# Optimization experiments

Hardware: AMD Instinct MI355X
Metric: run time of the kernel (lower is better)

## Reference

```python
import jax, jax.numpy as jnp
import numpy as np

N_NODES = 40000
N_EDGES = 640000
IN_CH = 128
HID_CH = 256
EDGE_DIM = 64
N_SAMP = 2048
T = 1.0
EPS_GIN = 0.0
EPS_NORM = 1e-12


def setup_inputs() -> dict:
    key = jax.random.key(0)
    ks = jax.random.split(key, 12)
    x = jax.random.normal(ks[0], (N_NODES, IN_CH), dtype=jnp.float32)
    edge_index = jax.random.randint(ks[1], (2, N_EDGES), 0, N_NODES, dtype=jnp.int64)
    edge_attr = jax.random.normal(ks[2], (N_EDGES, EDGE_DIM), dtype=jnp.float32)
    pos_ind = jax.random.randint(ks[3], (N_SAMP,), 0, N_NODES, dtype=jnp.int64)
    neg_ind = jax.random.randint(ks[4], (N_SAMP,), 0, N_NODES, dtype=jnp.int64)
    # GINEConv internal edge projection Linear(64 -> 128)
    We = jax.random.normal(ks[5], (EDGE_DIM, IN_CH), dtype=jnp.float32) / np.sqrt(EDGE_DIM)
    be = jnp.zeros((IN_CH,), dtype=jnp.float32)
    # MLP: Linear(128->256), ReLU, Linear(256->256)
    W1 = jax.random.normal(ks[6], (IN_CH, HID_CH), dtype=jnp.float32) / np.sqrt(IN_CH)
    b1 = jnp.zeros((HID_CH,), dtype=jnp.float32)
    W2 = jax.random.normal(ks[7], (HID_CH, HID_CH), dtype=jnp.float32) / np.sqrt(HID_CH)
    b2 = jnp.zeros((HID_CH,), dtype=jnp.float32)
    thresholding_node = jax.random.normal(ks[8], (1, HID_CH), dtype=jnp.float32)
    return {"x": x, "edge_index": edge_index, "edge_attr": edge_attr,
            "pos_ind": pos_ind, "neg_ind": neg_ind,
            "We": We, "be": be, "W1": W1, "b1": b1, "W2": W2, "b2": b2,
            "thresholding_node": thresholding_node}


def _normalize(v):
    n = jnp.linalg.norm(v, axis=-1, keepdims=True)
    return v / jnp.maximum(n, EPS_NORM)


def reference(x, edge_index, edge_attr, pos_ind, neg_ind,
              We, be, W1, b1, W2, b2, thresholding_node):
    src, dst = edge_index[0], edge_index[1]  # PyG: message from x_j (src) to target i (dst)
    edge_emb = edge_attr @ We + be                    # [E, in_ch]
    msg = jax.nn.relu(x[src] + edge_emb)              # gather + add + relu
    agg = jax.ops.segment_sum(msg, dst, num_segments=x.shape[0])  # scatter-add
    h = (1.0 + EPS_GIN) * x + agg
    emb = jax.nn.relu(h @ W1 + b1) @ W2 + b2          # [N, hid]

    center = _normalize(emb[0])                       # [hid]
    pos = _normalize(emb[pos_ind])                    # [P, hid]
    neg = _normalize(emb[neg_ind])                    # [Q, hid]
    thr = _normalize(thresholding_node)               # [1, hid]

    pos_score_mean = (center[None, :] * pos).sum(-1).mean(-1)
    neg_score_mean = (center[None, :] * neg).sum(-1).mean(-1)
    thr_score = (center * thr).sum(-1)                # [1]

    pos_loss = jnp.log(jnp.clip(jax.nn.sigmoid((pos_score_mean - thr_score) / T), 1e-12)).mean()
    neg_loss = jnp.log(jnp.clip(jax.nn.sigmoid((thr_score - neg_score_mean) / T), 1e-12)).mean()
    return -pos_loss - neg_loss
```

## Files before the change

kernel.cpp:

```cpp
#include <hip/hip_runtime.h>
#include <math.h>

#define N_NODES 40000
#define N_EDGES 640000
#define IN_CH 128
#define HID_CH 256
#define EDGE_DIM 64
#define N_SAMP 2048
#define NSEL (1 + 2 * N_SAMP)
#define MAXU 4097
#define HBUCKETS 5120

__global__ __launch_bounds__(256) void init_kernel(
    int* __restrict__ slot, int* __restrict__ counters,
    int* __restrict__ hist, float4* __restrict__ agg4)
{
    const int i = blockIdx.x * 256 + threadIdx.x;
    const int n = gridDim.x * 256;
    for (int j = i; j < 40960; j += n) slot[j] = -1;
    for (int j = i; j < HBUCKETS; j += n) hist[j] = 0;
    for (int j = i; j < 32; j += n) counters[j] = 0;
    const float4 z = make_float4(0.f, 0.f, 0.f, 0.f);
    for (int j = i; j < (MAXU * IN_CH) / 4; j += n) agg4[j] = z;
}

__global__ __launch_bounds__(256) void flag_kernel(
    const int* __restrict__ pos, const int* __restrict__ neg,
    int* __restrict__ slot, int* __restrict__ counters)
{
    int r = blockIdx.x * 256 + threadIdx.x;
    if (r >= NSEL) return;
    int node = (r == 0) ? 0 : (r <= N_SAMP ? pos[r - 1] : neg[r - 1 - N_SAMP]);
    int old = atomicCAS(&slot[node], -1, -2);
    if (old == -1) slot[node] = atomicAdd(&counters[1], 1);
}

__global__ __launch_bounds__(256) void compact_kernel(
    const int* __restrict__ ei, const int* __restrict__ slot,
    int* __restrict__ counters, int* __restrict__ hist, int4* __restrict__ cmp)
{
    const int tid = threadIdx.x, wave = tid >> 6, lane = tid & 63;
    const int e = blockIdx.x * 256 + tid;
    const int d = ei[N_EDGES + e];
    const int sl = slot[d];
    const bool valid = (sl >= 0);
    unsigned long long m = __ballot(valid);
    int wrank = __popcll(m & ((1ULL << lane) - 1ULL));
    __shared__ int woff[4];
    __shared__ int bbase;
    if (lane == 0) woff[wave] = __popcll(m);
    __syncthreads();
    if (tid == 0) {
        int t = 0;
        for (int i = 0; i < 4; ++i) { int c = woff[i]; woff[i] = t; t += c; }
        bbase = atomicAdd(&counters[0], t);
    }
    __syncthreads();
    if (valid) {
        int idx = bbase + woff[wave] + wrank;
        cmp[idx] = make_int4(e, ei[e], sl, 0);
        atomicAdd(&hist[sl], 1);
    }
}

__global__ __launch_bounds__(1024) void scan_kernel(
    const int* __restrict__ hist, int* __restrict__ cursor)
{
    __shared__ int tmp[1024];
    const int t = threadIdx.x;
    int v[5]; int s = 0;
#pragma unroll
    for (int i = 0; i < 5; ++i) { v[i] = hist[t * 5 + i]; s += v[i]; }
    tmp[t] = s;
    __syncthreads();
    for (int d = 1; d < 1024; d <<= 1) {
        int a = (t >= d) ? tmp[t - d] : 0;
        __syncthreads();
        tmp[t] += a;
        __syncthreads();
    }
    int run = tmp[t] - s;
#pragma unroll
    for (int i = 0; i < 5; ++i) { cursor[t * 5 + i] = run; run += v[i]; }
}

__global__ __launch_bounds__(256) void scatter_kernel(
    const int4* __restrict__ cmp, const int* __restrict__ counters,
    int* __restrict__ cursor, int4* __restrict__ sorted)
{
    const int M = counters[0];
    for (int i = blockIdx.x * 256 + threadIdx.x; i < M; i += gridDim.x * 256) {
        int4 c = cmp[i];
        int p = atomicAdd(&cursor[c.z], 1);
        sorted[p] = c;
    }
}

__global__ __launch_bounds__(256) void edge_kernel(
    const float* __restrict__ x, const float* __restrict__ edge_attr,
    const float* __restrict__ We, const float* __restrict__ be,
    const int* __restrict__ counters, const int4* __restrict__ sorted,
    float* __restrict__ agg_c)
{
    __shared__ float sWe[EDGE_DIM * IN_CH];
    __shared__ float sAttr[4][16 * EDGE_DIM];
    __shared__ int sE[4][16], sS[4][16], sL[4][16];
    const int tid = threadIdx.x, wave = tid >> 6, lane = tid & 63;
    const int M = counters[0];

    {
        const float4* s4 = (const float4*)We;
        float4* d4 = (float4*)sWe;
        for (int i = tid; i < (EDGE_DIM * IN_CH) / 4; i += 256) d4[i] = s4[i];
    }
    __syncthreads();
    const float be0 = be[lane], be1 = be[64 + lane];

    for (int b = blockIdx.x * 64; b < M; b += gridDim.x * 64) {
        const int wb = b + wave * 16;
        if (lane < 16) {
            int idx = wb + lane;
            bool v = idx < M;
            int4 c = sorted[v ? idx : 0];
            sE[wave][lane] = c.x;
            sS[wave][lane] = c.y;
            sL[wave][lane] = v ? c.z : -1;
        }
        __syncthreads();
        {
            int sub = lane >> 4, q = lane & 15;
#pragma unroll
            for (int p = 0; p < 4; ++p) {
                int j = p * 4 + sub;
                int e = sE[wave][j];
                ((float4*)&sAttr[wave][j * EDGE_DIM])[q] =
                    ((const float4*)(edge_attr + (size_t)e * EDGE_DIM))[q];
            }
        }
        __syncthreads();

        float acc0[16], acc1[16];
#pragma unroll
        for (int j = 0; j < 16; ++j) { acc0[j] = 0.f; acc1[j] = 0.f; }
        for (int k0 = 0; k0 < EDGE_DIM; k0 += 4) {
            float w0[4], w1[4];
#pragma unroll
            for (int kk = 0; kk < 4; ++kk) {
                w0[kk] = sWe[(k0 + kk) * IN_CH + lane];
                w1[kk] = sWe[(k0 + kk) * IN_CH + 64 + lane];
            }
#pragma unroll
            for (int j = 0; j < 16; ++j) {
                float4 a = *(const float4*)&sAttr[wave][j * EDGE_DIM + k0];
                acc0[j] += a.x * w0[0] + a.y * w0[1] + a.z * w0[2] + a.w * w0[3];
                acc1[j] += a.x * w1[0] + a.y * w1[1] + a.z * w1[2] + a.w * w1[3];
            }
        }

        float sum0 = 0.f, sum1 = 0.f;
#pragma unroll
        for (int j = 0; j < 16; ++j) {
            int sl = sL[wave][j];
            if (sl >= 0) {
                int s = sS[wave][j];
                float m0 = fmaxf(x[(size_t)s * IN_CH + lane] + acc0[j] + be0, 0.f);
                float m1 = fmaxf(x[(size_t)s * IN_CH + 64 + lane] + acc1[j] + be1, 0.f);
                sum0 += m0;
                sum1 += m1;
                bool flush = (j == 15) || (sL[wave][j + 1] != sl);
                if (flush) {
                    atomicAdd(&agg_c[(size_t)sl * IN_CH + lane], sum0);
                    atomicAdd(&agg_c[(size_t)sl * IN_CH + 64 + lane], sum1);
                    sum0 = 0.f;
                    sum1 = 0.f;
                }
            }
        }
        __syncthreads();
    }
}

__global__ __launch_bounds__(256) void mlp_kernel(
    const float* __restrict__ x, const float* __restrict__ agg_c,
    const int* __restrict__ slot, const int* __restrict__ pos,
    const int* __restrict__ neg, const float* __restrict__ W1,
    const float* __restrict__ b1, const float* __restrict__ W2,
    const float* __restrict__ b2, float* __restrict__ emb)
{
    __shared__ float sin_[16][IN_CH];
    __shared__ float shid[16][HID_CH];
    __shared__ int snode[16], sslot[16];
    const int tid = threadIdx.x;
    const int r0 = blockIdx.x * 16;
    if (tid < 16) {
        int r = r0 + tid;
        int node = 0;
        if (r < NSEL && r > 0) node = (r <= N_SAMP) ? pos[r - 1] : neg[r - 1 - N_SAMP];
        snode[tid] = node;
        sslot[tid] = slot[node];
    }
    __syncthreads();
    for (int i = tid; i < 16 * (IN_CH / 4); i += 256) {
        int rr = i >> 5, k4 = i & 31;
        int n = snode[rr], sl = sslot[rr];
        float4 xa = ((const float4*)(x + (size_t)n * IN_CH))[k4];
        float4 ga = ((const float4*)(agg_c + (size_t)sl * IN_CH))[k4];
        ((float4*)sin_[rr])[k4] =
            make_float4(xa.x + ga.x, xa.y + ga.y, xa.z + ga.z, xa.w + ga.w);
    }
    __syncthreads();

    float acc[16];
#pragma unroll
    for (int rr = 0; rr < 16; ++rr) acc[rr] = 0.f;
    for (int k0 = 0; k0 < IN_CH; k0 += 4) {
        float w[4];
#pragma unroll
        for (int kk = 0; kk < 4; ++kk) w[kk] = W1[(k0 + kk) * HID_CH + tid];
#pragma unroll
        for (int rr = 0; rr < 16; ++rr) {
            float4 h = *(const float4*)&sin_[rr][k0];
            acc[rr] += h.x * w[0] + h.y * w[1] + h.z * w[2] + h.w * w[3];
        }
    }
    float bb1 = b1[tid];
#pragma unroll
    for (int rr = 0; rr < 16; ++rr) shid[rr][tid] = fmaxf(acc[rr] + bb1, 0.f);
    __syncthreads();

#pragma unroll
    for (int rr = 0; rr < 16; ++rr) acc[rr] = 0.f;
    for (int k0 = 0; k0 < HID_CH; k0 += 4) {
        float w[4];
#pragma unroll
        for (int kk = 0; kk < 4; ++kk) w[kk] = W2[(k0 + kk) * HID_CH + tid];
#pragma unroll
        for (int rr = 0; rr < 16; ++rr) {
            float4 h = *(const float4*)&shid[rr][k0];
            acc[rr] += h.x * w[0] + h.y * w[1] + h.z * w[2] + h.w * w[3];
        }
    }
    float bb2 = b2[tid];
#pragma unroll
    for (int rr = 0; rr < 16; ++rr) {
        int r = r0 + rr;
        if (r < NSEL) emb[(size_t)r * HID_CH + tid] = acc[rr] + bb2;
    }
}

__global__ __launch_bounds__(256) void score_kernel(
    const float* __restrict__ emb, float* __restrict__ partial)
{
    const int tid = threadIdx.x;
    const int wave = tid >> 6, lane = tid & 63;
    const int rid = blockIdx.x * 4 + wave;
    const float4 c = ((const float4*)emb)[lane];
    const float4 v = ((const float4*)(emb + (size_t)(rid + 1) * HID_CH))[lane];
    float cc = c.x * c.x + c.y * c.y + c.z * c.z + c.w * c.w;
    float vv = v.x * v.x + v.y * v.y + v.z * v.z + v.w * v.w;
    float cv = c.x * v.x + c.y * v.y + c.z * v.z + c.w * v.w;
#pragma unroll
    for (int off = 32; off; off >>= 1) {
        cc += __shfl_xor(cc, off, 64);
        vv += __shfl_xor(vv, off, 64);
        cv += __shfl_xor(cv, off, 64);
    }
    float score = cv / (fmaxf(sqrtf(cc), 1e-12f) * fmaxf(sqrtf(vv), 1e-12f));
    __shared__ float wsum[4];
    if (lane == 0) wsum[wave] = score;
    __syncthreads();
    if (tid == 0) partial[blockIdx.x] = wsum[0] + wsum[1] + wsum[2] + wsum[3];
}

__global__ __launch_bounds__(64) void loss_kernel(
    const float* __restrict__ emb, const float* __restrict__ thrn,
    const float* __restrict__ partial, float* __restrict__ out)
{
    const int lane = threadIdx.x;
    const float4 c = ((const float4*)emb)[lane];
    const float4 t = ((const float4*)thrn)[lane];
    float cc = c.x * c.x + c.y * c.y + c.z * c.z + c.w * c.w;
    float tt = t.x * t.x + t.y * t.y + t.z * t.z + t.w * t.w;
    float ct = c.x * t.x + c.y * t.y + c.z * t.z + c.w * t.w;
    float ps = 0.f, ns = 0.f;
#pragma unroll
    for (int i = 0; i < 8; ++i) ps += partial[lane + 64 * i];
#pragma unroll
    for (int i = 0; i < 8; ++i) ns += partial[512 + lane + 64 * i];
#pragma unroll
    for (int off = 32; off; off >>= 1) {
        cc += __shfl_xor(cc, off, 64);
        tt += __shfl_xor(tt, off, 64);
        ct += __shfl_xor(ct, off, 64);
        ps += __shfl_xor(ps, off, 64);
        ns += __shfl_xor(ns, off, 64);
    }
    if (lane == 0) {
        float thr = ct / (fmaxf(sqrtf(cc), 1e-12f) * fmaxf(sqrtf(tt), 1e-12f));
        float pm = ps / (float)N_SAMP;
        float nm = ns / (float)N_SAMP;
        float s1 = 1.f / (1.f + expf(-(pm - thr)));
        float s2 = 1.f / (1.f + expf(-(thr - nm)));
        s1 = fmaxf(s1, 1e-12f);
        s2 = fmaxf(s2, 1e-12f);
        out[0] = -(logf(s1) + logf(s2));
    }
}

extern "C" void kernel_launch(void* const* d_in, const int* in_sizes, int n_in,
                              void* d_out, int out_size, void* d_ws, size_t ws_size,
                              hipStream_t stream)
{
    const float* x         = (const float*)d_in[0];
    const int*   ei        = (const int*)d_in[1];
    const float* edge_attr = (const float*)d_in[2];
    const int*   pos       = (const int*)d_in[3];
    const int*   neg       = (const int*)d_in[4];
    const float* We        = (const float*)d_in[5];
    const float* be        = (const float*)d_in[6];
    const float* W1        = (const float*)d_in[7];
    const float* b1        = (const float*)d_in[8];
    const float* W2        = (const float*)d_in[9];
    const float* b2        = (const float*)d_in[10];
    const float* thrn      = (const float*)d_in[11];
    float* out = (float*)d_out;

    int* slot     = (int*)d_ws;
    int* counters = slot + 40960;
    int* hist     = counters + 32;
    int* cursor   = hist + HBUCKETS;
    int4* cmp     = (int4*)(cursor + HBUCKETS);
    int4* sorted  = cmp + N_EDGES;
    float* agg_c  = (float*)(sorted + N_EDGES);
    float* emb    = agg_c + 524800;
    float* partial= emb + 1048832;

    init_kernel<<<512, 256, 0, stream>>>(slot, counters, hist, (float4*)agg_c);
    flag_kernel<<<(NSEL + 255) / 256, 256, 0, stream>>>(pos, neg, slot, counters);
    compact_kernel<<<N_EDGES / 256, 256, 0, stream>>>(ei, slot, counters, hist, cmp);
    scan_kernel<<<1, 1024, 0, stream>>>(hist, cursor);
    scatter_kernel<<<256, 256, 0, stream>>>(cmp, counters, cursor, sorted);
    edge_kernel<<<1024, 256, 0, stream>>>(x, edge_attr, We, be, counters, sorted, agg_c);
    mlp_kernel<<<(NSEL + 15) / 16, 256, 0, stream>>>(x, agg_c, slot, pos, neg,
                                                     W1, b1, W2, b2, emb);
    score_kernel<<<1024, 256, 0, stream>>>(emb, partial);
    loss_kernel<<<1, 64, 0, stream>>>(emb, thrn, partial, out);
}
```

Baseline: 367.4 us.

## Fuse pipeline into one cooperative persistent kernel and drop edge sorting

After: 919.1 us. 2.5x slower.

```diff
diff --git a/kernel.cpp b/kernel.cpp
--- a/kernel.cpp
+++ b/kernel.cpp
@@ -1,5 +1,8 @@
 #include <hip/hip_runtime.h>
+#include <hip/hip_cooperative_groups.h>
 #include <math.h>
+
+namespace cg = cooperative_groups;
 
 #define N_NODES 40000
 #define N_EDGES 640000
@@ -9,301 +12,270 @@
 #define N_SAMP 2048
 #define NSEL (1 + 2 * N_SAMP)
 #define MAXU 4097
-#define HBUCKETS 5120
-
-__global__ __launch_bounds__(256) void init_kernel(
-    int* __restrict__ slot, int* __restrict__ counters,
-    int* __restrict__ hist, float4* __restrict__ agg4)
+#define GRID 512
+#define BLK 256
+
+struct EdgeSmem {
+    float sWe[EDGE_DIM * IN_CH];
+    float sAttr[4][16 * EDGE_DIM];
+    int sE[4][16], sS[4][16], sL[4][16];
+};
+struct MlpSmem {
+    float sin_[16][IN_CH];
+    float shid[16][HID_CH];
+    int snode[16], sslot[16];
+};
+struct CmpSmem { int woff[4]; int bbase; };
+struct ScSmem { float wsum[4]; };
+
+__global__ __launch_bounds__(BLK) void mega_kernel(
+    const float* __restrict__ x, const int* __restrict__ ei,
+    const float* __restrict__ edge_attr,
+    const int* __restrict__ pos, const int* __restrict__ neg,
+    const float* __restrict__ We, const float* __restrict__ be,
+    const float* __restrict__ W1, const float* __restrict__ b1,
+    const float* __restrict__ W2, const float* __restrict__ b2,
+    const float* __restrict__ thrn,
+    int* slot, int* counters, int4* cmp, float* agg_c,
+    float* emb, float* partial, float* out)
 {
-    const int i = blockIdx.x * 256 + threadIdx.x;
-    const int n = gridDim.x * 256;
-    for (int j = i; j < 40960; j += n) slot[j] = -1;
-    for (int j = i; j < HBUCKETS; j += n) hist[j] = 0;
-    for (int j = i; j < 32; j += n) counters[j] = 0;
-    const float4 z = make_float4(0.f, 0.f, 0.f, 0.f);
-    for (int j = i; j < (MAXU * IN_CH) / 4; j += n) agg4[j] = z;
-}
-
-__global__ __launch_bounds__(256) void flag_kernel(
-    const int* __restrict__ pos, const int* __restrict__ neg,
-    int* __restrict__ slot, int* __restrict__ counters)
-{
-    int r = blockIdx.x * 256 + threadIdx.x;
-    if (r >= NSEL) return;
-    int node = (r == 0) ? 0 : (r <= N_SAMP ? pos[r - 1] : neg[r - 1 - N_SAMP]);
-    int old = atomicCAS(&slot[node], -1, -2);
-    if (old == -1) slot[node] = atomicAdd(&counters[1], 1);
-}
-
-__global__ __launch_bounds__(256) void compact_kernel(
-    const int* __restrict__ ei, const int* __restrict__ slot,
-    int* __restrict__ counters, int* __restrict__ hist, int4* __restrict__ cmp)
-{
+    cg::grid_group grid = cg::this_grid();
+    __shared__ __align__(16) char smem[sizeof(EdgeSmem)];
     const int tid = threadIdx.x, wave = tid >> 6, lane = tid & 63;
-    const int e = blockIdx.x * 256 + tid;
-    const int d = ei[N_EDGES + e];
-    const int sl = slot[d];
-    const bool valid = (sl >= 0);
-    unsigned long long m = __ballot(valid);
-    int wrank = __popcll(m & ((1ULL << lane) - 1ULL));
-    __shared__ int woff[4];
-    __shared__ int bbase;
-    if (lane == 0) woff[wave] = __popcll(m);
-    __syncthreads();
-    if (tid == 0) {
-        int t = 0;
-        for (int i = 0; i < 4; ++i) { int c = woff[i]; woff[i] = t; t += c; }
-        bbase = atomicAdd(&counters[0], t);
-    }
-    __syncthreads();
-    if (valid) {
-        int idx = bbase + woff[wave] + wrank;
-        cmp[idx] = make_int4(e, ei[e], sl, 0);
-        atomicAdd(&hist[sl], 1);
-    }
-}
-
-__global__ __launch_bounds__(1024) void scan_kernel(
-    const int* __restrict__ hist, int* __restrict__ cursor)
-{
-    __shared__ int tmp[1024];
-    const int t = threadIdx.x;
-    int v[5]; int s = 0;
-#pragma unroll
-    for (int i = 0; i < 5; ++i) { v[i] = hist[t * 5 + i]; s += v[i]; }
-    tmp[t] = s;
-    __syncthreads();
-    for (int d = 1; d < 1024; d <<= 1) {
-        int a = (t >= d) ? tmp[t - d] : 0;
+    const int gtid = blockIdx.x * BLK + tid;
+    const int gsz = GRID * BLK;
+
+    for (int j = gtid; j < 40960; j += gsz) slot[j] = -1;
+    if (gtid < 32) counters[gtid] = 0;
+    {
+        float4* agg4 = (float4*)agg_c;
+        const float4 z = make_float4(0.f, 0.f, 0.f, 0.f);
+        for (int j = gtid; j < (MAXU * IN_CH) / 4; j += gsz) agg4[j] = z;
+    }
+    __threadfence();
+    grid.sync();
+
+    for (int r = gtid; r < NSEL; r += gsz) {
+        int node = (r == 0) ? 0 : (r <= N_SAMP ? pos[r - 1] : neg[r - 1 - N_SAMP]);
+        int old = atomicCAS(&slot[node], -1, -2);
+        if (old == -1) slot[node] = atomicAdd(&counters[1], 1);
+    }
+    __threadfence();
+    grid.sync();
+
+    {
+        CmpSmem* cs = (CmpSmem*)smem;
+        for (int base = blockIdx.x * BLK; base < N_EDGES; base += gsz) {
+            int e = base + tid;
+            int d = ei[N_EDGES + e];
+            int sl = slot[d];
+            bool valid = (sl >= 0);
+            unsigned long long m = __ballot(valid);
+            int wrank = __popcll(m & ((1ULL << lane) - 1ULL));
+            if (lane == 0) cs->woff[wave] = __popcll(m);
+            __syncthreads();
+            if (tid == 0) {
+                int t = 0;
+                for (int i = 0; i < 4; ++i) { int c = cs->woff[i]; cs->woff[i] = t; t += c; }
+                cs->bbase = atomicAdd(&counters[0], t);
+            }
+            __syncthreads();
+            if (valid) cmp[cs->bbase + cs->woff[wave] + wrank] = make_int4(e, ei[e], sl, 0);
+            __syncthreads();
+        }
+    }
+    __threadfence();
+    grid.sync();
+
+    {
+        EdgeSmem* es = (EdgeSmem*)smem;
+        const int M = counters[0];
+        {
+            const float4* s4 = (const float4*)We;
+            float4* d4 = (float4*)es->sWe;
+            for (int i = tid; i < (EDGE_DIM * IN_CH) / 4; i += BLK) d4[i] = s4[i];
+        }
         __syncthreads();
-        tmp[t] += a;
-        __syncthreads();
-    }
-    int run = tmp[t] - s;
-#pragma unroll
-    for (int i = 0; i < 5; ++i) { cursor[t * 5 + i] = run; run += v[i]; }
-}
-
-__global__ __launch_bounds__(256) void scatter_kernel(
-    const int4* __restrict__ cmp, const int* __restrict__ counters,
-    int* __restrict__ cursor, int4* __restrict__ sorted)
-{
-    const int M = counters[0];
-    for (int i = blockIdx.x * 256 + threadIdx.x; i < M; i += gridDim.x * 256) {
-        int4 c = cmp[i];
-        int p = atomicAdd(&cursor[c.z], 1);
-        sorted[p] = c;
-    }
-}
-
-__global__ __launch_bounds__(256) void edge_kernel(
-    const float* __restrict__ x, const float* __restrict__ edge_attr,
-    const float* __restrict__ We, const float* __restrict__ be,
-    const int* __restrict__ counters, const int4* __restrict__ sorted,
-    float* __restrict__ agg_c)
-{
-    __shared__ float sWe[EDGE_DIM * IN_CH];
-    __shared__ float sAttr[4][16 * EDGE_DIM];
-    __shared__ int sE[4][16], sS[4][16], sL[4][16];
-    const int tid = threadIdx.x, wave = tid >> 6, lane = tid & 63;
-    const int M = counters[0];
-
-    {
-        const float4* s4 = (const float4*)We;
-        float4* d4 = (float4*)sWe;
-        for (int i = tid; i < (EDGE_DIM * IN_CH) / 4; i += 256) d4[i] = s4[i];
-    }
-    __syncthreads();
-    const float be0 = be[lane], be1 = be[64 + lane];
-
-    for (int b = blockIdx.x * 64; b < M; b += gridDim.x * 64) {
-        const int wb = b + wave * 16;
-        if (lane < 16) {
-            int idx = wb + lane;
-            bool v = idx < M;
-            int4 c = sorted[v ? idx : 0];
-            sE[wave][lane] = c.x;
-            sS[wave][lane] = c.y;
-            sL[wave][lane] = v ? c.z : -1;
-        }
-        __syncthreads();
-        {
-            int sub = lane >> 4, q = lane & 15;
-#pragma unroll
-            for (int p = 0; p < 4; ++p) {
-                int j = p * 4 + sub;
-                int e = sE[wave][j];
-                ((float4*)&sAttr[wave][j * EDGE_DIM])[q] =
-                    ((const float4*)(edge_attr + (size_t)e * EDGE_DIM))[q];
-            }
-        }
-        __syncthreads();
-
-        float acc0[16], acc1[16];
-#pragma unroll
-        for (int j = 0; j < 16; ++j) { acc0[j] = 0.f; acc1[j] = 0.f; }
-        for (int k0 = 0; k0 < EDGE_DIM; k0 += 4) {
-            float w0[4], w1[4];
-#pragma unroll
-            for (int kk = 0; kk < 4; ++kk) {
-                w0[kk] = sWe[(k0 + kk) * IN_CH + lane];
-                w1[kk] = sWe[(k0 + kk) * IN_CH + 64 + lane];
+        const float be0 = be[lane], be1 = be[64 + lane];
+
+        for (int b = blockIdx.x * 64; b < M; b += GRID * 64) {
+            const int wb = b + wave * 16;
+            if (lane < 16) {
+                int idx = wb + lane;
+                bool v = idx < M;
+                int4 c = cmp[v ? idx : 0];
+                es->sE[wave][lane] = c.x;
+                es->sS[wave][lane] = c.y;
+                es->sL[wave][lane] = v ? c.z : -1;
+            }
+            __syncthreads();
+            {
+                int sub = lane >> 4, q = lane & 15;
+#pragma unroll
+                for (int p = 0; p < 4; ++p) {
+                    int j = p * 4 + sub;
+                    int e = es->sE[wave][j];
+                    ((float4*)&es->sAttr[wave][j * EDGE_DIM])[q] =
+                        ((const float4*)(edge_attr + (size_t)e * EDGE_DIM))[q];
+                }
+            }
+            __syncthreads();
+
+            float acc0[16], acc1[16];
+#pragma unroll
+            for (int j = 0; j < 16; ++j) { acc0[j] = 0.f; acc1[j] = 0.f; }
+            for (int k0 = 0; k0 < EDGE_DIM; k0 += 4) {
+                float w0[4], w1[4];
+#pragma unroll
+                for (int kk = 0; kk < 4; ++kk) {
+                    w0[kk] = es->sWe[(k0 + kk) * IN_CH + lane];
+                    w1[kk] = es->sWe[(k0 + kk) * IN_CH + 64 + lane];
+                }
+#pragma unroll
+                for (int j = 0; j < 16; ++j) {
+                    float4 a = *(const float4*)&es->sAttr[wave][j * EDGE_DIM + k0];
+                    acc0[j] += a.x * w0[0] + a.y * w0[1] + a.z * w0[2] + a.w * w0[3];
+                    acc1[j] += a.x * w1[0] + a.y * w1[1] + a.z * w1[2] + a.w * w1[3];
+                }
             }
 #pragma unroll
             for (int j = 0; j < 16; ++j) {
-                float4 a = *(const float4*)&sAttr[wave][j * EDGE_DIM + k0];
-                acc0[j] += a.x * w0[0] + a.y * w0[1] + a.z * w0[2] + a.w * w0[3];
-                acc1[j] += a.x * w1[0] + a.y * w1[1] + a.z * w1[2] + a.w * w1[3];
-            }
-        }
-
-        float sum0 = 0.f, sum1 = 0.f;
-#pragma unroll
-        for (int j = 0; j < 16; ++j) {
-            int sl = sL[wave][j];
-            if (sl >= 0) {
-                int s = sS[wave][j];
-                float m0 = fmaxf(x[(size_t)s * IN_CH + lane] + acc0[j] + be0, 0.f);
-                float m1 = fmaxf(x[(size_t)s * IN_CH + 64 + lane] + acc1[j] + be1, 0.f);
-                sum0 += m0;
-                sum1 += m1;
-                bool flush = (j == 15) || (sL[wave][j + 1] != sl);
-                if (flush) {
-                    atomicAdd(&agg_c[(size_t)sl * IN_CH + lane], sum0);
-                    atomicAdd(&agg_c[(size_t)sl * IN_CH + 64 + lane], sum1);
-                    sum0 = 0.f;
-                    sum1 = 0.f;
-                }
-            }
-        }
-        __syncthreads();
-    }
-}
-
-__global__ __launch_bounds__(256) void mlp_kernel(
-    const float* __restrict__ x, const float* __restrict__ agg_c,
-    const int* __restrict__ slot, const int* __restrict__ pos,
-    const int* __restrict__ neg, const float* __restrict__ W1,
-    const float* __restrict__ b1, const float* __restrict__ W2,
-    const float* __restrict__ b2, float* __restrict__ emb)
-{
-    __shared__ float sin_[16][IN_CH];
-    __shared__ float shid[16][HID_CH];
-    __shared__ int snode[16], sslot[16];
-    const int tid = threadIdx.x;
-    const int r0 = blockIdx.x * 16;
-    if (tid < 16) {
-        int r = r0 + tid;
-        int node = 0;
-        if (r < NSEL && r > 0) node = (r <= N_SAMP) ? pos[r - 1] : neg[r - 1 - N_SAMP];
-        snode[tid] = node;
-        sslot[tid] = slot[node];
-    }
-    __syncthreads();
-    for (int i = tid; i < 16 * (IN_CH / 4); i += 256) {
-        int rr = i >> 5, k4 = i & 31;
-        int n = snode[rr], sl = sslot[rr];
-        float4 xa = ((const float4*)(x + (size_t)n * IN_CH))[k4];
-        float4 ga = ((const float4*)(agg_c + (size_t)sl * IN_CH))[k4];
-        ((float4*)sin_[rr])[k4] =
-            make_float4(xa.x + ga.x, xa.y + ga.y, xa.z + ga.z, xa.w + ga.w);
-    }
-    __syncthreads();
-
-    float acc[16];
-#pragma unroll
-    for (int rr = 0; rr < 16; ++rr) acc[rr] = 0.f;
-    for (int k0 = 0; k0 < IN_CH; k0 += 4) {
-        float w[4];
-#pragma unroll
-        for (int kk = 0; kk < 4; ++kk) w[kk] = W1[(k0 + kk) * HID_CH + tid];
-#pragma unroll
-        for (int rr = 0; rr < 16; ++rr) {
-            float4 h = *(const float4*)&sin_[rr][k0];
-            acc[rr] += h.x * w[0] + h.y * w[1] + h.z * w[2] + h.w * w[3];
-        }
-    }
-    float bb1 = b1[tid];
-#pragma unroll
-    for (int rr = 0; rr < 16; ++rr) shid[rr][tid] = fmaxf(acc[rr] + bb1, 0.f);
-    __syncthreads();
-
-#pragma unroll
-    for (int rr = 0; rr < 16; ++rr) acc[rr] = 0.f;
-    for (int k0 = 0; k0 < HID_CH; k0 += 4) {
-        float w[4];
-#pragma unroll
-        for (int kk = 0; kk < 4; ++kk) w[kk] = W2[(k0 + kk) * HID_CH + tid];
-#pragma unroll
-        for (int rr = 0; rr < 16; ++rr) {
-            float4 h = *(const float4*)&shid[rr][k0];
-            acc[rr] += h.x * w[0] + h.y * w[1] + h.z * w[2] + h.w * w[3];
-        }
-    }
-    float bb2 = b2[tid];
-#pragma unroll
-    for (int rr = 0; rr < 16; ++rr) {
-        int r = r0 + rr;
-        if (r < NSEL) emb[(size_t)r * HID_CH + tid] = acc[rr] + bb2;
-    }
-}
-
-__global__ __launch_bounds__(256) void score_kernel(
-    const float* __restrict__ emb, float* __restrict__ partial)
-{
-    const int tid = threadIdx.x;
-    const int wave = tid >> 6, lane = tid & 63;
-    const int rid = blockIdx.x * 4 + wave;
-    const float4 c = ((const float4*)emb)[lane];
-    const float4 v = ((const float4*)(emb + (size_t)(rid + 1) * HID_CH))[lane];
-    float cc = c.x * c.x + c.y * c.y + c.z * c.z + c.w * c.w;
-    float vv = v.x * v.x + v.y * v.y + v.z * v.z + v.w * v.w;
-    float cv = c.x * v.x + c.y * v.y + c.z * v.z + c.w * v.w;
-#pragma unroll
-    for (int off = 32; off; off >>= 1) {
-        cc += __shfl_xor(cc, off, 64);
-        vv += __shfl_xor(vv, off, 64);
-        cv += __shfl_xor(cv, off, 64);
-    }
-    float score = cv / (fmaxf(sqrtf(cc), 1e-12f) * fmaxf(sqrtf(vv), 1e-12f));
-    __shared__ float wsum[4];
-    if (lane == 0) wsum[wave] = score;
-    __syncthreads();
-    if (tid == 0) partial[blockIdx.x] = wsum[0] + wsum[1] + wsum[2] + wsum[3];
-}
-
-__global__ __launch_bounds__(64) void loss_kernel(
-    const float* __restrict__ emb, const float* __restrict__ thrn,
-    const float* __restrict__ partial, float* __restrict__ out)
-{
-    const int lane = threadIdx.x;
-    const float4 c = ((const float4*)emb)[lane];
-    const float4 t = ((const float4*)thrn)[lane];
-    float cc = c.x * c.x + c.y * c.y + c.z * c.z + c.w * c.w;
-    float tt = t.x * t.x + t.y * t.y + t.z * t.z + t.w * t.w;
-    float ct = c.x * t.x + c.y * t.y + c.z * t.z + c.w * t.w;
-    float ps = 0.f, ns = 0.f;
-#pragma unroll
-    for (int i = 0; i < 8; ++i) ps += partial[lane + 64 * i];
-#pragma unroll
-    for (int i = 0; i < 8; ++i) ns += partial[512 + lane + 64 * i];
-#pragma unroll
-    for (int off = 32; off; off >>= 1) {
-        cc += __shfl_xor(cc, off, 64);
-        tt += __shfl_xor(tt, off, 64);
-        ct += __shfl_xor(ct, off, 64);
-        ps += __shfl_xor(ps, off, 64);
-        ns += __shfl_xor(ns, off, 64);
-    }
-    if (lane == 0) {
-        float thr = ct / (fmaxf(sqrtf(cc), 1e-12f) * fmaxf(sqrtf(tt), 1e-12f));
-        float pm = ps / (float)N_SAMP;
-        float nm = ns / (float)N_SAMP;
-        float s1 = 1.f / (1.f + expf(-(pm - thr)));
-        float s2 = 1.f / (1.f + expf(-(thr - nm)));
-        s1 = fmaxf(s1, 1e-12f);
-        s2 = fmaxf(s2, 1e-12f);
-        out[0] = -(logf(s1) + logf(s2));
+                int sl = es->sL[wave][j];
+                if (sl >= 0) {
+                    int s = es->sS[wave][j];
+                    float m0 = fmaxf(x[(size_t)s * IN_CH + lane] + acc0[j] + be0, 0.f);
+                    float m1 = fmaxf(x[(size_t)s * IN_CH + 64 + lane] + acc1[j] + be1, 0.f);
+                    atomicAdd(&agg_c[(size_t)sl * IN_CH + lane], m0);
+                    atomicAdd(&agg_c[(size_t)sl * IN_CH + 64 + lane], m1);
+                }
+            }
+            __syncthreads();
+        }
+    }
+    __threadfence();
+    grid.sync();
+
+    {
+        MlpSmem* ms = (MlpSmem*)smem;
+        for (int tile = blockIdx.x; tile * 16 < NSEL; tile += GRID) {
+            const int r0 = tile * 16;
+            if (tid < 16) {
+                int r = r0 + tid;
+                int node = 0;
+                if (r < NSEL && r > 0)
+                    node = (r <= N_SAMP) ? pos[r - 1] : neg[r - 1 - N_SAMP];
+                ms->snode[tid] = node;
+                ms->sslot[tid] = slot[node];
+            }
+            __syncthreads();
+            for (int i = tid; i < 16 * (IN_CH / 4); i += BLK) {
+                int rr = i >> 5, k4 = i & 31;
+                int n = ms->snode[rr], sl = ms->sslot[rr];
+                float4 xa = ((const float4*)(x + (size_t)n * IN_CH))[k4];
+                float4 ga = ((const float4*)(agg_c + (size_t)sl * IN_CH))[k4];
+                ((float4*)ms->sin_[rr])[k4] =
+                    make_float4(xa.x + ga.x, xa.y + ga.y, xa.z + ga.z, xa.w + ga.w);
+            }
+            __syncthreads();
+
+            float acc[16];
+#pragma unroll
+            for (int rr = 0; rr < 16; ++rr) acc[rr] = 0.f;
+            for (int k0 = 0; k0 < IN_CH; k0 += 4) {
+                float w[4];
+#pragma unroll
+                for (int kk = 0; kk < 4; ++kk) w[kk] = W1[(k0 + kk) * HID_CH + tid];
+#pragma unroll
+                for (int rr = 0; rr < 16; ++rr) {
+                    float4 h = *(const float4*)&ms->sin_[rr][k0];
+                    acc[rr] += h.x * w[0] + h.y * w[1] + h.z * w[2] + h.w * w[3];
+                }
+            }
+            float bb1 = b1[tid];
+#pragma unroll
+            for (int rr = 0; rr < 16; ++rr) ms->shid[rr][tid] = fmaxf(acc[rr] + bb1, 0.f);
+            __syncthreads();
+
+#pragma unroll
+            for (int rr = 0; rr < 16; ++rr) acc[rr] = 0.f;
+            for (int k0 = 0; k0 < HID_CH; k0 += 4) {
+                float w[4];
+#pragma unroll
+                for (int kk = 0; kk < 4; ++kk) w[kk] = W2[(k0 + kk) * HID_CH + tid];
+#pragma unroll
+                for (int rr = 0; rr < 16; ++rr) {
+                    float4 h = *(const float4*)&ms->shid[rr][k0];
+                    acc[rr] += h.x * w[0] + h.y * w[1] + h.z * w[2] + h.w * w[3];
+                }
+            }
+            float bb2 = b2[tid];
+#pragma unroll
+            for (int rr = 0; rr < 16; ++rr) {
+                int r = r0 + rr;
+                if (r < NSEL) emb[(size_t)r * HID_CH + tid] = acc[rr] + bb2;
+            }
+            __syncthreads();
+        }
+    }
+    __threadfence();
+    grid.sync();
+
+    {
+        ScSmem* ss = (ScSmem*)smem;
+        const float4 c = ((const float4*)emb)[lane];
+        float cc = c.x * c.x + c.y * c.y + c.z * c.z + c.w * c.w;
+        for (int sb = blockIdx.x; sb < 1024; sb += GRID) {
+            const int rid = sb * 4 + wave;
+            const float4 v = ((const float4*)(emb + (size_t)(rid + 1) * HID_CH))[lane];
+            float vv = v.x * v.x + v.y * v.y + v.z * v.z + v.w * v.w;
+            float cv = c.x * v.x + c.y * v.y + c.z * v.z + c.w * v.w;
+            float ccr = cc;
+#pragma unroll
+            for (int off = 32; off; off >>= 1) {
+                ccr += __shfl_xor(ccr, off, 64);
+                vv += __shfl_xor(vv, off, 64);
+                cv += __shfl_xor(cv, off, 64);
+            }
+            float score = cv / (fmaxf(sqrtf(ccr), 1e-12f) * fmaxf(sqrtf(vv), 1e-12f));
+            if (lane == 0) ss->wsum[wave] = score;
+            __syncthreads();
+            if (tid == 0)
+                partial[sb] = ss->wsum[0] + ss->wsum[1] + ss->wsum[2] + ss->wsum[3];
+            __syncthreads();
+        }
+    }
+    __threadfence();
+    grid.sync();
+
+    if (blockIdx.x == 0 && tid < 64) {
+        const float4 c = ((const float4*)emb)[lane];
+        const float4 t = ((const float4*)thrn)[lane];
+        float cc = c.x * c.x + c.y * c.y + c.z * c.z + c.w * c.w;
+        float tt = t.x * t.x + t.y * t.y + t.z * t.z + t.w * t.w;
+        float ct = c.x * t.x + c.y * t.y + c.z * t.z + c.w * t.w;
+        float ps = 0.f, ns = 0.f;
+#pragma unroll
+        for (int i = 0; i < 8; ++i) ps += partial[lane + 64 * i];
+#pragma unroll
+        for (int i = 0; i < 8; ++i) ns += partial[512 + lane + 64 * i];
+#pragma unroll
+        for (int off = 32; off; off >>= 1) {
+            cc += __shfl_xor(cc, off, 64);
+            tt += __shfl_xor(tt, off, 64);
+            ct += __shfl_xor(ct, off, 64);
+            ps += __shfl_xor(ps, off, 64);
+            ns += __shfl_xor(ns, off, 64);
+        }
+        if (lane == 0) {
+            float thr = ct / (fmaxf(sqrtf(cc), 1e-12f) * fmaxf(sqrtf(tt), 1e-12f));
+            float pm = ps / (float)N_SAMP;
+            float nm = ns / (float)N_SAMP;
+            float s1 = 1.f / (1.f + expf(-(pm - thr)));
+            float s2 = 1.f / (1.f + expf(-(thr - nm)));
+            s1 = fmaxf(s1, 1e-12f);
+            s2 = fmaxf(s2, 1e-12f);
+            out[0] = -(logf(s1) + logf(s2));
+        }
     }
 }
 
@@ -327,22 +299,16 @@
 
     int* slot     = (int*)d_ws;
     int* counters = slot + 40960;
-    int* hist     = counters + 32;
-    int* cursor   = hist + HBUCKETS;
-    int4* cmp     = (int4*)(cursor + HBUCKETS);
-    int4* sorted  = cmp + N_EDGES;
-    float* agg_c  = (float*)(sorted + N_EDGES);
+    int4* cmp     = (int4*)(counters + 32);
+    float* agg_c  = (float*)(cmp + N_EDGES);
     float* emb    = agg_c + 524800;
-    float* partial= emb + 1048832;
-
-    init_kernel<<<512, 256, 0, stream>>>(slot, counters, hist, (float4*)agg_c);
-    flag_kernel<<<(NSEL + 255) / 256, 256, 0, stream>>>(pos, neg, slot, counters);
-    compact_kernel<<<N_EDGES / 256, 256, 0, stream>>>(ei, slot, counters, hist, cmp);
-    scan_kernel<<<1, 1024, 0, stream>>>(hist, cursor);
-    scatter_kernel<<<256, 256, 0, stream>>>(cmp, counters, cursor, sorted);
-    edge_kernel<<<1024, 256, 0, stream>>>(x, edge_attr, We, be, counters, sorted, agg_c);
-    mlp_kernel<<<(NSEL + 15) / 16, 256, 0, stream>>>(x, agg_c, slot, pos, neg,
-                                                     W1, b1, W2, b2, emb);
-    score_kernel<<<1024, 256, 0, stream>>>(emb, partial);
-    loss_kernel<<<1, 64, 0, stream>>>(emb, thrn, partial, out);
+    float* partial = emb + 1048832;
+
+    void* args[] = {
+        (void*)&x, (void*)&ei, (void*)&edge_attr, (void*)&pos, (void*)&neg,
+        (void*)&We, (void*)&be, (void*)&W1, (void*)&b1, (void*)&W2, (void*)&b2,
+        (void*)&thrn, (void*)&slot, (void*)&counters, (void*)&cmp, (void*)&agg_c,
+        (void*)&emb, (void*)&partial, (void*)&out};
+    hipLaunchCooperativeKernel((void*)mega_kernel, dim3(GRID), dim3(BLK),
+                               args, 0, stream);
 }
```
